# Performance work log

Hardware: AMD Instinct MI355X
Metric: run time of the kernel (lower is better)

## Reference

```python
import jax, jax.numpy as jnp
import numpy as np

# dims: P patches, D=N_azi*N_ele directions, R=P*D radiances, E COO edges,
# T echogram samples, F rfft bins
P, D, R, E, T, NOBJ = 128, 128, 16384, 131072, 1024, 8
F = T // 2 + 1
SR, C_SOUND = 16000.0, 343.0
LOG_GAMMA = float(np.log(1e-3))   # fsm_gamma = 0.001
AIR = 1e-3                        # air absorption coefficient
BOUNCES = 4                       # truncated num_bounces


def setup_inputs():
    key = jax.random.key(0)
    ks = jax.random.split(key, 11)
    return {
        "source_pos": jax.random.normal(ks[0], (3,), jnp.float32) * 2.0,
        "receiver_pos": jax.random.normal(ks[1], (3,), jnp.float32) * 2.0,
        "absorption": jax.random.uniform(ks[2], (NOBJ,), jnp.float32, minval=0.05, maxval=0.6),
        "scattering": jax.random.uniform(ks[3], (NOBJ,), jnp.float32, minval=0.1, maxval=0.9),
        "gk_val": jax.random.uniform(ks[4], (E,), jnp.float32) * 0.1,            # form factors
        "local_kernel_basis": jax.random.uniform(ks[5], (2, D, D), jnp.float32) / D,  # [brdf,Dout,Din]
        "average_distance": jax.random.uniform(ks[6], (R,), jnp.float32) * 10.0 + 1.0,  # meters
        "radiance_pos": jax.random.normal(ks[7], (R, 3), jnp.float32) * 5.0,
        "gk_row": jax.random.randint(ks[8], (E,), 0, R),
        "gk_col": jax.random.randint(ks[9], (E,), 0, R),
        "object_ids": jax.random.randint(ks[10], (P,), 0, NOBJ),
    }


def _path_factor(dist):
    """Frequency-domain factor for a propagation path of length dist [N] -> [N,F].
    Combines fractional delay phase, FSM exponential window gamma^(tau_sec),
    and air absorption exp(-alpha*dist)."""
    freqs = jnp.arange(F, dtype=jnp.float32)
    tau = dist * (SR / C_SOUND)  # delay in samples
    phase = jnp.exp((-2j * np.pi / T) * tau[:, None] * freqs[None, :])
    decay = jnp.exp((LOG_GAMMA / C_SOUND - AIR) * dist)  # fsm + air, per path
    return phase * decay[:, None].astype(phase.dtype)


def reference(source_pos, receiver_pos, absorption, scattering, gk_val,
              local_kernel_basis, average_distance, radiance_pos,
              gk_row, gk_col, object_ids):
    # --- injection: source -> patch-direction radiance [R,F] ---
    d_src = jnp.linalg.norm(radiance_pos - source_pos[None, :], axis=-1)
    g_src = 1.0 / (d_src * d_src + 1e-3)
    rad = g_src[:, None] * _path_factor(d_src)  # complex [R,F]

    # --- BRDF-factorized local kernel: K[p] = sum_b c[b,p] * B[b] ---
    refl = 1.0 - absorption                                   # [NOBJ]
    coeff = jnp.stack([refl * scattering, refl * (1.0 - scattering)])  # [2,NOBJ]
    c_patch = coeff[:, object_ids]                            # [2,P]
    K = jnp.einsum('bp,bde->pde', c_patch, local_kernel_basis)  # [P,Dout,Din]

    prop = _path_factor(average_distance)  # per-radiance transport delay/decay [R,F]

    def bounce(r):
        r = r.reshape(P, D, F)
        r = jnp.einsum('pde,pef->pdf', K.astype(jnp.complex64), r)  # local direction mixing
        r = r.reshape(R, F) * prop
        # sparse COO global kernel: out[row] += val * r[col]
        return jax.ops.segment_sum(gk_val[:, None] * r[gk_col], gk_row, num_segments=R)

    total = rad
    r = rad
    for _ in range(BOUNCES):
        r = bounce(r)
        total = total + r

    # --- detection: patch-direction radiance -> receiver echogram ---
    d_rec = jnp.linalg.norm(radiance_pos - receiver_pos[None, :], axis=-1)
    w_rec = 1.0 / (d_rec * d_rec + 1e-3)
    echo_f = jnp.sum(w_rec[:, None] * _path_factor(d_rec) * total, axis=0)  # [F]

    # FSM correction: divide out the exponential window in time domain
    t = jnp.arange(T, dtype=jnp.float32) / SR
    fsm_window = jnp.exp(LOG_GAMMA * t)
    echogram = jnp.fft.irfft(echo_f, n=T) / fsm_window
    return echogram
```

## Files before the change

### kernel.cpp

```cpp
#include <hip/hip_runtime.h>
#include <math.h>

#define PP 128
#define DD 128
#define RR 16384
#define EE 131072
#define TT 1024
#define FF 513
#define FP 520
#define FPITCH 1056
#define NRB 1024
#define PSTRIDE 528
#define EPITCH 136

#define TAU_SCALE 46.64723032069971
#define KDECAY   -0.0211392282f
#define LOG_GAMMA -6.907755278982137f
#define TWO_PI    6.283185307179586

typedef __attribute__((ext_vector_type(8))) short bf16x8;
typedef __attribute__((ext_vector_type(4))) float f32x4;
typedef unsigned short u16;

__device__ __forceinline__ u16 f2bf(float x) {
    unsigned u = __float_as_uint(x);
    unsigned r = (u + 0x7fffu + ((u >> 16) & 1u)) >> 16;
    return (u16)r;
}
__device__ __forceinline__ float bf2f(u16 b) {
    return __uint_as_float(((unsigned)b) << 16);
}

__device__ __forceinline__ void pf_sincos(float tau, int f, float* s, float* c) {
    int ti = (int)tau;
    float tf = tau - (float)ti;
    int m = (ti * f) & 1023;
    float u = fmaf(tf, (float)f, (float)m);
    float ang = u * -0.006135923151542565f;
    __sincosf(ang, s, c);
}

__global__ void k_per_row(const float* __restrict__ rpos,
                          const float* __restrict__ spos,
                          const float* __restrict__ cpos,
                          const float* __restrict__ avg_dist,
                          float* __restrict__ per_row) {
    int r = blockIdx.x * blockDim.x + threadIdx.x;
    if (r >= RR) return;
    float x = rpos[3*r], y = rpos[3*r+1], z = rpos[3*r+2];

    float dx = x - spos[0], dy = y - spos[1], dz = z - spos[2];
    float ds = sqrtf(dx*dx + dy*dy + dz*dz);
    per_row[0*RR + r] = (1.0f/(ds*ds + 0.001f)) * expf(KDECAY * ds);
    per_row[1*RR + r] = ds * (float)TAU_SCALE;

    dx = x - cpos[0]; dy = y - cpos[1]; dz = z - cpos[2];
    float dr = sqrtf(dx*dx + dy*dy + dz*dz);
    per_row[2*RR + r] = (1.0f/(dr*dr + 0.001f)) * expf(KDECAY * dr);
    per_row[3*RR + r] = dr * (float)TAU_SCALE;

    float da = avg_dist[r];
    per_row[4*RR + r] = expf(KDECAY * da);
    per_row[5*RR + r] = da * (float)TAU_SCALE;
}

__global__ void k_build_K(const float* __restrict__ absorption,
                          const float* __restrict__ scattering,
                          const int* __restrict__ object_ids,
                          const float* __restrict__ basis,
                          float* __restrict__ Kmat) {
    int idx = blockIdx.x * 256 + threadIdx.x;
    int p  = idx >> 14;
    int de = idx & 16383;
    int obj = object_ids[p];
    float refl = 1.0f - absorption[obj];
    float sc   = scattering[obj];
    Kmat[idx] = refl*sc*basis[de] + refl*(1.0f - sc)*basis[16384 + de];
}

__global__ void k_count(const int* __restrict__ gk_row, int* __restrict__ counts) {
    int e = blockIdx.x * 256 + threadIdx.x;
    atomicAdd(&counts[gk_row[e]], 1);
}

__global__ __launch_bounds__(1024) void k_scan(const int* __restrict__ counts,
                                               int* __restrict__ row_start,
                                               int* __restrict__ cursor) {
    __shared__ int sh[1024];
    int tid = threadIdx.x;
    int base = tid * 16;
    int local[16];
    int sum = 0;
    #pragma unroll
    for (int j = 0; j < 16; j++) { local[j] = sum; sum += counts[base + j]; }
    sh[tid] = sum;
    __syncthreads();
    for (int off = 1; off < 1024; off <<= 1) {
        int v = (tid >= off) ? sh[tid - off] : 0;
        __syncthreads();
        sh[tid] += v;
        __syncthreads();
    }
    int chunk_excl = sh[tid] - sum;
    #pragma unroll
    for (int j = 0; j < 16; j++) {
        int v = chunk_excl + local[j];
        row_start[base + j] = v;
        cursor[base + j] = v;
    }
    if (tid == 1023) row_start[RR] = chunk_excl + sum;
}

__global__ void k_scatter(const int* __restrict__ gk_row,
                          const float* __restrict__ gk_val,
                          const int* __restrict__ gk_col,
                          int* __restrict__ cursor,
                          int2* __restrict__ edge) {
    int e = blockIdx.x * 256 + threadIdx.x;
    int pos = atomicAdd(&cursor[gk_row[e]], 1);
    edge[pos] = make_int2(gk_col[e], __float_as_int(gk_val[e]));
}

__global__ __launch_bounds__(256) void k_init(const float* __restrict__ per_row,
                                              u16* __restrict__ cur,
                                              float* __restrict__ echo) {
    __shared__ float2 sh[4][64][9];
    int fl = threadIdx.x & 63, rg = threadIdx.x >> 6;
    int r0 = blockIdx.x * 32;
    float2 eacc[9];
    #pragma unroll
    for (int k = 0; k < 9; k++) eacc[k] = make_float2(0.f, 0.f);

    for (int i = 0; i < 8; i++) {
        int r = r0 + rg + i * 4;
        float amp = per_row[r],      tau  = per_row[RR + r];
        float w   = per_row[2*RR+r], taur = per_row[3*RR + r];
        float s1, c1, rs1, rc1, s2, c2, rs2, rc2;
        pf_sincos(tau,  fl, &s1, &c1);  pf_sincos(tau,  64, &rs1, &rc1);
        pf_sincos(taur, fl, &s2, &c2);  pf_sincos(taur, 64, &rs2, &rc2);
        u16* wrow = cur + (size_t)r * FPITCH;
        #pragma unroll
        for (int k = 0; k < 9; k++) {
            int f = fl + (k << 6);
            float re = amp * c1, im = amp * s1;
            if (f < FP)
                *(unsigned*)(wrow + f * 2) =
                    (unsigned)f2bf(re) | ((unsigned)f2bf(im) << 16);
            if (f < FF) {
                eacc[k].x = fmaf(w, c2*re - s2*im, eacc[k].x);
                eacc[k].y = fmaf(w, c2*im + s2*re, eacc[k].y);
            }
            float n1c = c1*rc1 - s1*rs1, n1s = s1*rc1 + c1*rs1;
            c1 = n1c; s1 = n1s;
            float n2c = c2*rc2 - s2*rs2, n2s = s2*rc2 + c2*rs2;
            c2 = n2c; s2 = n2s;
        }
    }
    #pragma unroll
    for (int k = 0; k < 9; k++) sh[rg][fl][k] = eacc[k];
    __syncthreads();
    if (rg == 0) {
        #pragma unroll
        for (int k = 0; k < 9; k++) {
            int f = fl + (k << 6);
            if (f < FF) {
                float sx = sh[0][fl][k].x + sh[1][fl][k].x + sh[2][fl][k].x + sh[3][fl][k].x;
                float sy = sh[0][fl][k].y + sh[1][fl][k].y + sh[2][fl][k].y + sh[3][fl][k].y;
                atomicAdd(&echo[2*f],   sx);
                atomicAdd(&echo[2*f+1], sy);
            }
        }
    }
}

__global__ __launch_bounds__(256) void k_matmul(const float* __restrict__ Kmat,
                                                const u16* __restrict__ in,
                                                const float* __restrict__ per_row,
                                                u16* __restrict__ out) {
    __shared__ u16 vlds[2][16 * EPITCH];
    int b = blockIdx.x;
    int xcd = b & 7;
    int g = b >> 3;
    int p = (g >> 3) * 8 + xcd;
    int nq = g & 7;
    int nt0 = nq * 8;
    int ntEnd = (nq == 7) ? 65 : nt0 + 8;

    int tid  = threadIdx.x;
    int wave = tid >> 6;
    int lane = tid & 63;
    int quad = lane >> 4;
    int n    = lane & 15;
    int mt0  = wave << 1;

    bf16x8 Ah[2][4], Al[2][4];
    #pragma unroll
    for (int mi = 0; mi < 2; mi++) {
        const float* kp = Kmat + (p << 14) + ((mt0 + mi) * 16 + n) * 128 + quad * 8;
        #pragma unroll
        for (int kt = 0; kt < 4; kt++) {
            float4 x0 = *(const float4*)(kp + kt * 32);
            float4 x1 = *(const float4*)(kp + kt * 32 + 4);
            float xs[8] = {x0.x,x0.y,x0.z,x0.w,x1.x,x1.y,x1.z,x1.w};
            bf16x8 h, l;
            #pragma unroll
            for (int j = 0; j < 8; j++) {
                u16 hb = f2bf(xs[j]);
                h[j] = (short)hb;
                l[j] = (short)f2bf(xs[j] - bf2f(hb));
            }
            Ah[mi][kt] = h; Al[mi][kt] = l;
        }
    }
    float dec_[2][4];
    float pc[2][4], ps[2][4];
    float rc[2][4], rs[2][4];
    int fq = (n >> 1);
    #pragma unroll
    for (int mi = 0; mi < 2; mi++)
        #pragma unroll
        for (int r = 0; r < 4; r++) {
            int row = (p << 7) + (mt0 + mi) * 16 + quad * 4 + r;
            dec_[mi][r] = per_row[4*RR + row];
            float tau = per_row[5*RR + row];
            pf_sincos(tau, nt0 * 8 + fq, &ps[mi][r], &pc[mi][r]);
            pf_sincos(tau, 8, &rs[mi][r], &rc[mi][r]);
        }

    const u16* pin = in + (size_t)(p << 7) * FPITCH;
    uint4 pk;
    int se = tid >> 1, sc8 = (tid & 1) << 3;
    auto loadTile = [&](int nt) {
        pk = *(const uint4*)(pin + (size_t)se * FPITCH + nt * 16 + sc8);
    };
    auto writeTile = [&](int buf) {
        u16* dst = &vlds[buf][0];
        unsigned w[4] = {pk.x, pk.y, pk.z, pk.w};
        #pragma unroll
        for (int j = 0; j < 8; j++) {
            u16 v = (u16)(w[j >> 1] >> ((j & 1) * 16));
            dst[(sc8 + j) * EPITCH + se] = v;
        }
    };

    loadTile(nt0); writeTile(0);
    for (int nt = nt0; nt < ntEnd; nt++) {
        int cb = (nt - nt0) & 1;
        __syncthreads();
        if (nt + 1 < ntEnd) { loadTile(nt + 1); writeTile(cb ^ 1); }

        f32x4 acc0 = {0.f,0.f,0.f,0.f}, acc1 = {0.f,0.f,0.f,0.f};
        const u16* vb = &vlds[cb][n * EPITCH];
        #pragma unroll
        for (int kt = 0; kt < 4; kt++) {
            bf16x8 Bh = *(const bf16x8*)(vb + kt * 32 + quad * 8);
            acc0 = __builtin_amdgcn_mfma_f32_16x16x32_bf16(Ah[0][kt], Bh, acc0, 0,0,0);
            acc1 = __builtin_amdgcn_mfma_f32_16x16x32_bf16(Ah[1][kt], Bh, acc1, 0,0,0);
            acc0 = __builtin_amdgcn_mfma_f32_16x16x32_bf16(Al[0][kt], Bh, acc0, 0,0,0);
            acc1 = __builtin_amdgcn_mfma_f32_16x16x32_bf16(Al[1][kt], Bh, acc1, 0,0,0);
        }

        int nfl = nt * 16 + n;
        bool odd = nfl & 1;
        #pragma unroll
        for (int mi = 0; mi < 2; mi++) {
            f32x4 a = mi ? acc1 : acc0;
            #pragma unroll
            for (int r = 0; r < 4; r++) {
                float av = a[r];
                float pv = __shfl_xor(av, 1);
                float s = ps[mi][r], c = pc[mi][r];
                float o = dec_[mi][r] * (odd ? fmaf(av, c,  s*pv)
                                             : fmaf(av, c, -s*pv));
                int row = (p << 7) + (mt0 + mi) * 16 + quad * 4 + r;
                out[(size_t)row * FPITCH + nfl] = f2bf(o);
                float nc = c*rc[mi][r] - s*rs[mi][r];
                float nsv = s*rc[mi][r] + c*rs[mi][r];
                pc[mi][r] = nc; ps[mi][r] = nsv;
            }
        }
    }
}

__global__ __launch_bounds__(512) void k_segsum(const int* __restrict__ row_start,
                                                const int2* __restrict__ edge,
                                                const u16* __restrict__ in,
                                                u16* __restrict__ outp,
                                                const float* __restrict__ per_row,
                                                float2* __restrict__ part,
                                                int store_cur) {
    __shared__ float2 sh[4][128][5];
    int rb = blockIdx.x;
    int fl = threadIdx.x & 127, ry = threadIdx.x >> 7;
    bool tail = (fl < 8);
    float2 e0 = {0.f,0.f}, e1 = {0.f,0.f}, e2 = {0.f,0.f}, e3 = {0.f,0.f}, e4 = {0.f,0.f};

    for (int i = 0; i < 4; i++) {
        int row = (rb << 4) + (ry << 2) + i;
        int s0 = row_start[row], s1 = row_start[row + 1];
        float a0r=0.f,a0i=0.f,a1r=0.f,a1i=0.f,a2r=0.f,a2i=0.f,a3r=0.f,a3i=0.f;
        float t4r=0.f,t4i=0.f;
        int t = s0;
        for (; t + 1 < s1; t += 2) {
            int2 ed0 = edge[t], ed1 = edge[t+1];
            float v0 = __int_as_float(ed0.y), v1 = __int_as_float(ed1.y);
            const u16* g0p = in + (size_t)ed0.x * FPITCH + (fl << 1);
            const u16* g1p = in + (size_t)ed1.x * FPITCH + (fl << 1);
            unsigned b00 = *(const unsigned*)(g0p);
            unsigned b01 = *(const unsigned*)(g0p + 256);
            unsigned b02 = *(const unsigned*)(g0p + 512);
            unsigned b03 = *(const unsigned*)(g0p + 768);
            unsigned b10 = *(const unsigned*)(g1p);
            unsigned b11 = *(const unsigned*)(g1p + 256);
            unsigned b12 = *(const unsigned*)(g1p + 512);
            unsigned b13 = *(const unsigned*)(g1p + 768);
            a0r = fmaf(v0, bf2f((u16)(b00 & 0xffffu)), a0r); a0i = fmaf(v0, bf2f((u16)(b00 >> 16)), a0i);
            a1r = fmaf(v0, bf2f((u16)(b01 & 0xffffu)), a1r); a1i = fmaf(v0, bf2f((u16)(b01 >> 16)), a1i);
            a2r = fmaf(v0, bf2f((u16)(b02 & 0xffffu)), a2r); a2i = fmaf(v0, bf2f((u16)(b02 >> 16)), a2i);
            a3r = fmaf(v0, bf2f((u16)(b03 & 0xffffu)), a3r); a3i = fmaf(v0, bf2f((u16)(b03 >> 16)), a3i);
            a0r = fmaf(v1, bf2f((u16)(b10 & 0xffffu)), a0r); a0i = fmaf(v1, bf2f((u16)(b10 >> 16)), a0i);
            a1r = fmaf(v1, bf2f((u16)(b11 & 0xffffu)), a1r); a1i = fmaf(v1, bf2f((u16)(b11 >> 16)), a1i);
            a2r = fmaf(v1, bf2f((u16)(b12 & 0xffffu)), a2r); a2i = fmaf(v1, bf2f((u16)(b12 >> 16)), a2i);
            a3r = fmaf(v1, bf2f((u16)(b13 & 0xffffu)), a3r); a3i = fmaf(v1, bf2f((u16)(b13 >> 16)), a3i);
            if (tail) {
                unsigned b04 = *(const unsigned*)(g0p + 1024);
                unsigned b14 = *(const unsigned*)(g1p + 1024);
                t4r = fmaf(v0, bf2f((u16)(b04 & 0xffffu)), t4r); t4i = fmaf(v0, bf2f((u16)(b04 >> 16)), t4i);
                t4r = fmaf(v1, bf2f((u16)(b14 & 0xffffu)), t4r); t4i = fmaf(v1, bf2f((u16)(b14 >> 16)), t4i);
            }
        }
        if (t < s1) {
            int2 ed = edge[t];
            float v = __int_as_float(ed.y);
            const u16* g = in + (size_t)ed.x * FPITCH + (fl << 1);
            unsigned b0 = *(const unsigned*)(g);
            unsigned b1 = *(const unsigned*)(g + 256);
            unsigned b2 = *(const unsigned*)(g + 512);
            unsigned b3 = *(const unsigned*)(g + 768);
            a0r = fmaf(v, bf2f((u16)(b0 & 0xffffu)), a0r); a0i = fmaf(v, bf2f((u16)(b0 >> 16)), a0i);
            a1r = fmaf(v, bf2f((u16)(b1 & 0xffffu)), a1r); a1i = fmaf(v, bf2f((u16)(b1 >> 16)), a1i);
            a2r = fmaf(v, bf2f((u16)(b2 & 0xffffu)), a2r); a2i = fmaf(v, bf2f((u16)(b2 >> 16)), a2i);
            a3r = fmaf(v, bf2f((u16)(b3 & 0xffffu)), a3r); a3i = fmaf(v, bf2f((u16)(b3 >> 16)), a3i);
            if (tail) {
                unsigned b4 = *(const unsigned*)(g + 1024);
                t4r = fmaf(v, bf2f((u16)(b4 & 0xffffu)), t4r); t4i = fmaf(v, bf2f((u16)(b4 >> 16)), t4i);
            }
        }
        if (store_cur) {
            u16* w = outp + (size_t)row * FPITCH + (fl << 1);
            *(unsigned*)(w)       = (unsigned)f2bf(a0r) | ((unsigned)f2bf(a0i) << 16);
            *(unsigned*)(w + 256) = (unsigned)f2bf(a1r) | ((unsigned)f2bf(a1i) << 16);
            *(unsigned*)(w + 512) = (unsigned)f2bf(a2r) | ((unsigned)f2bf(a2i) << 16);
            *(unsigned*)(w + 768) = (unsigned)f2bf(a3r) | ((unsigned)f2bf(a3i) << 16);
            if (tail)
                *(unsigned*)(w + 1024) = (unsigned)f2bf(t4r) | ((unsigned)f2bf(t4i) << 16);
        }
        float wr = per_row[2*RR + row], taur = per_row[3*RR + row];
        float s, c;
        pf_sincos(taur, fl, &s, &c);
        e0.x = fmaf(wr, c*a0r - s*a0i, e0.x); e0.y = fmaf(wr, c*a0i + s*a0r, e0.y);
        pf_sincos(taur, fl + 128, &s, &c);
        e1.x = fmaf(wr, c*a1r - s*a1i, e1.x); e1.y = fmaf(wr, c*a1i + s*a1r, e1.y);
        pf_sincos(taur, fl + 256, &s, &c);
        e2.x = fmaf(wr, c*a2r - s*a2i, e2.x); e2.y = fmaf(wr, c*a2i + s*a2r, e2.y);
        pf_sincos(taur, fl + 384, &s, &c);
        e3.x = fmaf(wr, c*a3r - s*a3i, e3.x); e3.y = fmaf(wr, c*a3i + s*a3r, e3.y);
        if (tail && (512 + fl) < FF) {
            pf_sincos(taur, 512 + fl, &s, &c);
            e4.x = fmaf(wr, c*t4r - s*t4i, e4.x); e4.y = fmaf(wr, c*t4i + s*t4r, e4.y);
        }
    }
    sh[ry][fl][0] = e0; sh[ry][fl][1] = e1; sh[ry][fl][2] = e2;
    sh[ry][fl][3] = e3; sh[ry][fl][4] = e4;
    __syncthreads();
    if (ry == 0) {
        float2* pp = part + (size_t)rb * PSTRIDE;
        #pragma unroll
        for (int sidx = 0; sidx < 5; sidx++) {
            int fidx = sidx * 128 + fl;
            if (fidx < FP) {
                float2 v0 = sh[0][fl][sidx], v1 = sh[1][fl][sidx];
                float2 v2 = sh[2][fl][sidx], v3 = sh[3][fl][sidx];
                float2 acc = pp[fidx];
                acc.x += v0.x + v1.x + v2.x + v3.x;
                acc.y += v0.y + v1.y + v2.y + v3.y;
                pp[fidx] = acc;
            }
        }
    }
}

__global__ __launch_bounds__(256) void k_fold(const float2* __restrict__ part,
                                              float* __restrict__ echo) {
    int f = blockIdx.x;
    float sx = 0.f, sy = 0.f;
    for (int rb = threadIdx.x; rb < NRB; rb += 256) {
        float2 v = part[(size_t)rb * PSTRIDE + f];
        sx += v.x; sy += v.y;
    }
    for (int off = 32; off >= 1; off >>= 1) {
        sx += __shfl_down(sx, off, 64);
        sy += __shfl_down(sy, off, 64);
    }
    __shared__ float red[2][4];
    int lane = threadIdx.x & 63, w = threadIdx.x >> 6;
    if (lane == 0) { red[0][w] = sx; red[1][w] = sy; }
    __syncthreads();
    if (threadIdx.x == 0) {
        sx = red[0][0]+red[0][1]+red[0][2]+red[0][3];
        sy = red[1][0]+red[1][1]+red[1][2]+red[1][3];
        echo[2*f] += sx;
        echo[2*f+1] += sy;
    }
}

__global__ void k_irfft(const float* __restrict__ echo, float* __restrict__ out) {
    int t = blockIdx.x * blockDim.x + threadIdx.x;
    float acc = echo[0];
    float nyq = echo[2 * 512];
    acc += (t & 1) ? -nyq : nyq;
    for (int f = 1; f < 512; f++) {
        int m = (f * t) & 1023;
        float ang = (float)m * 0.006135923151542565f;
        float s, c; __sincosf(ang, &s, &c);
        acc += 2.0f * (echo[2*f]*c - echo[2*f+1]*s);
    }
    acc *= (1.0f / 1024.0f);
    float tsec = (float)t * (1.0f / 16000.0f);
    float win = expf(LOG_GAMMA * tsec);
    out[t] = acc / win;
}

extern "C" void kernel_launch(void* const* d_in, const int* in_sizes, int n_in,
                              void* d_out, int out_size, void* d_ws, size_t ws_size,
                              hipStream_t stream) {
    const float* source_pos   = (const float*)d_in[0];
    const float* receiver_pos = (const float*)d_in[1];
    const float* absorption   = (const float*)d_in[2];
    const float* scattering   = (const float*)d_in[3];
    const float* gk_val       = (const float*)d_in[4];
    const float* basis        = (const float*)d_in[5];
    const float* avg_dist     = (const float*)d_in[6];
    const float* rpos         = (const float*)d_in[7];
    const int*   gk_row       = (const int*)d_in[8];
    const int*   gk_col       = (const int*)d_in[9];
    const int*   object_ids   = (const int*)d_in[10];
    float* out = (float*)d_out;

    char* base = (char*)d_ws;
    size_t off = 0;
    auto alloc = [&](size_t bytes) -> void* {
        void* ptr = base + off;
        off = (off + bytes + 255) & ~(size_t)255;
        return ptr;
    };
    const size_t PLANE = (size_t)RR * FPITCH + FPITCH;
    float*  Kmat      = (float*)alloc(sizeof(float) * PP * DD * DD);
    u16*    cur       = (u16*)alloc(sizeof(u16) * PLANE);
    u16*    nxt       = (u16*)alloc(sizeof(u16) * PLANE);
    float*  per_row   = (float*)alloc(sizeof(float) * 6 * RR);
    int*    counts    = (int*)alloc(sizeof(int) * RR);
    int*    row_start = (int*)alloc(sizeof(int) * (RR + 1));
    int*    cursor    = (int*)alloc(sizeof(int) * RR);
    int2*   edge      = (int2*)alloc(sizeof(int2) * EE);
    float2* part      = (float2*)alloc(sizeof(float2) * NRB * PSTRIDE);
    float*  echo      = (float*)alloc(sizeof(float) * 1056);

    hipMemsetAsync(counts, 0, sizeof(int) * RR, stream);
    hipMemsetAsync(echo, 0, sizeof(float) * 1056, stream);
    hipMemsetAsync(part, 0, sizeof(float2) * NRB * PSTRIDE, stream);

    k_per_row<<<RR / 256, 256, 0, stream>>>(rpos, source_pos, receiver_pos, avg_dist, per_row);
    k_build_K<<<(PP * DD * DD) / 256, 256, 0, stream>>>(absorption, scattering, object_ids, basis, Kmat);
    k_count<<<EE / 256, 256, 0, stream>>>(gk_row, counts);
    k_scan<<<1, 1024, 0, stream>>>(counts, row_start, cursor);
    k_scatter<<<EE / 256, 256, 0, stream>>>(gk_row, gk_val, gk_col, cursor, edge);
    k_init<<<512, 256, 0, stream>>>(per_row, cur, echo);

    for (int b = 0; b < 4; b++) {
        k_matmul<<<1024, 256, 0, stream>>>(Kmat, cur, per_row, nxt);
        k_segsum<<<NRB, 512, 0, stream>>>(row_start, edge, nxt, cur,
                                          per_row, part, (b < 3) ? 1 : 0);
    }

    k_fold<<<FF, 256, 0, stream>>>(part, echo);
    k_irfft<<<4, 256, 0, stream>>>(echo, out);
}
```

Before: 485.3 us.

## Degree-sort rows for segsum, split frequencies across blocks, double-tile matmul stages

Rows are bucketed by edge count (histogram, scan, scatter), and the segment-sum kernel walks them in that order so rows with similar work share a block. Each block now covers 128 rows and one 64-bin slice of frequencies, where it used to cover 16 rows across all bins. NRB drops to 128, which shrinks the partials buffer and the fold work. The matmul kernel stages two N-tiles per barrier to halve synchronisations. This adds three small setup kernels, narrower per-thread gathers, and a serial 32-row shared reduction per block.

```diff
diff --git a/kernel.cpp b/kernel.cpp
--- a/kernel.cpp
+++ b/kernel.cpp
@@ -9,7 +9,7 @@
 #define FF 513
 #define FP 520
 #define FPITCH 1056
-#define NRB 1024
+#define NRB 128
 #define PSTRIDE 528
 #define EPITCH 136
 
@@ -121,6 +121,27 @@
     edge[pos] = make_int2(gk_col[e], __float_as_int(gk_val[e]));
 }
 
+__global__ void k_hist(const int* __restrict__ counts, int* __restrict__ bins) {
+    int r = blockIdx.x * 256 + threadIdx.x;
+    int c = counts[r]; if (c > 255) c = 255;
+    atomicAdd(&bins[c], 1);
+}
+__global__ __launch_bounds__(256) void k_binscan(const int* __restrict__ bins,
+                                                 int* __restrict__ bin_cursor) {
+    int t = threadIdx.x;
+    int s = 0;
+    for (int c = t + 1; c < 256; c++) s += bins[c];
+    bin_cursor[t] = s;
+}
+__global__ void k_scatter_rows(const int* __restrict__ counts,
+                               int* __restrict__ bin_cursor,
+                               int* __restrict__ row_order) {
+    int r = blockIdx.x * 256 + threadIdx.x;
+    int c = counts[r]; if (c > 255) c = 255;
+    int pos = atomicAdd(&bin_cursor[c], 1);
+    row_order[pos] = r;
+}
+
 __global__ __launch_bounds__(256) void k_init(const float* __restrict__ per_row,
                                               u16* __restrict__ cur,
                                               float* __restrict__ echo) {
@@ -177,7 +198,7 @@
                                                 const u16* __restrict__ in,
                                                 const float* __restrict__ per_row,
                                                 u16* __restrict__ out) {
-    __shared__ u16 vlds[2][16 * EPITCH];
+    __shared__ u16 vlds[2][32 * EPITCH];
     int b = blockIdx.x;
     int xcd = b & 7;
     int g = b >> 3;
@@ -185,6 +206,7 @@
     int nq = g & 7;
     int nt0 = nq * 8;
     int ntEnd = (nq == 7) ? 65 : nt0 + 8;
+    int nStages = (ntEnd - nt0 + 1) >> 1;
 
     int tid  = threadIdx.x;
     int wave = tid >> 6;
@@ -228,55 +250,62 @@
         }
 
     const u16* pin = in + (size_t)(p << 7) * FPITCH;
-    uint4 pk;
-    int se = tid >> 1, sc8 = (tid & 1) << 3;
-    auto loadTile = [&](int nt) {
-        pk = *(const uint4*)(pin + (size_t)se * FPITCH + nt * 16 + sc8);
+    uint4 pk0, pk1;
+    int se = tid >> 1, sc16 = (tid & 1) << 4;
+    auto loadStage = [&](int st) {
+        const u16* src = pin + (size_t)se * FPITCH + (nt0 + 2*st) * 16 + sc16;
+        pk0 = *(const uint4*)(src);
+        pk1 = *(const uint4*)(src + 8);
     };
-    auto writeTile = [&](int buf) {
+    auto writeStage = [&](int buf) {
         u16* dst = &vlds[buf][0];
-        unsigned w[4] = {pk.x, pk.y, pk.z, pk.w};
-        #pragma unroll
-        for (int j = 0; j < 8; j++) {
+        unsigned w[8] = {pk0.x, pk0.y, pk0.z, pk0.w, pk1.x, pk1.y, pk1.z, pk1.w};
+        #pragma unroll
+        for (int j = 0; j < 16; j++) {
             u16 v = (u16)(w[j >> 1] >> ((j & 1) * 16));
-            dst[(sc8 + j) * EPITCH + se] = v;
+            dst[(sc16 + j) * EPITCH + se] = v;
         }
     };
 
-    loadTile(nt0); writeTile(0);
-    for (int nt = nt0; nt < ntEnd; nt++) {
-        int cb = (nt - nt0) & 1;
+    loadStage(0); writeStage(0);
+    for (int st = 0; st < nStages; st++) {
+        int cb = st & 1;
         __syncthreads();
-        if (nt + 1 < ntEnd) { loadTile(nt + 1); writeTile(cb ^ 1); }
-
-        f32x4 acc0 = {0.f,0.f,0.f,0.f}, acc1 = {0.f,0.f,0.f,0.f};
-        const u16* vb = &vlds[cb][n * EPITCH];
-        #pragma unroll
-        for (int kt = 0; kt < 4; kt++) {
-            bf16x8 Bh = *(const bf16x8*)(vb + kt * 32 + quad * 8);
-            acc0 = __builtin_amdgcn_mfma_f32_16x16x32_bf16(Ah[0][kt], Bh, acc0, 0,0,0);
-            acc1 = __builtin_amdgcn_mfma_f32_16x16x32_bf16(Ah[1][kt], Bh, acc1, 0,0,0);
-            acc0 = __builtin_amdgcn_mfma_f32_16x16x32_bf16(Al[0][kt], Bh, acc0, 0,0,0);
-            acc1 = __builtin_amdgcn_mfma_f32_16x16x32_bf16(Al[1][kt], Bh, acc1, 0,0,0);
-        }
-
-        int nfl = nt * 16 + n;
-        bool odd = nfl & 1;
-        #pragma unroll
-        for (int mi = 0; mi < 2; mi++) {
-            f32x4 a = mi ? acc1 : acc0;
+        if (st + 1 < nStages) { loadStage(st + 1); writeStage(cb ^ 1); }
+
+        #pragma unroll
+        for (int sub = 0; sub < 2; sub++) {
+            int nt = nt0 + 2*st + sub;
+            if (nt >= ntEnd) break;
+            f32x4 acc0 = {0.f,0.f,0.f,0.f}, acc1 = {0.f,0.f,0.f,0.f};
+            const u16* vb = &vlds[cb][(n + (sub << 4)) * EPITCH];
             #pragma unroll
-            for (int r = 0; r < 4; r++) {
-                float av = a[r];
-                float pv = __shfl_xor(av, 1);
-                float s = ps[mi][r], c = pc[mi][r];
-                float o = dec_[mi][r] * (odd ? fmaf(av, c,  s*pv)
-                                             : fmaf(av, c, -s*pv));
-                int row = (p << 7) + (mt0 + mi) * 16 + quad * 4 + r;
-                out[(size_t)row * FPITCH + nfl] = f2bf(o);
-                float nc = c*rc[mi][r] - s*rs[mi][r];
-                float nsv = s*rc[mi][r] + c*rs[mi][r];
-                pc[mi][r] = nc; ps[mi][r] = nsv;
+            for (int kt = 0; kt < 4; kt++) {
+                bf16x8 Bh = *(const bf16x8*)(vb + kt * 32 + quad * 8);
+                acc0 = __builtin_amdgcn_mfma_f32_16x16x32_bf16(Ah[0][kt], Bh, acc0, 0,0,0);
+                acc1 = __builtin_amdgcn_mfma_f32_16x16x32_bf16(Ah[1][kt], Bh, acc1, 0,0,0);
+                acc0 = __builtin_amdgcn_mfma_f32_16x16x32_bf16(Al[0][kt], Bh, acc0, 0,0,0);
+                acc1 = __builtin_amdgcn_mfma_f32_16x16x32_bf16(Al[1][kt], Bh, acc1, 0,0,0);
+            }
+
+            int nfl = nt * 16 + n;
+            bool odd = nfl & 1;
+            #pragma unroll
+            for (int mi = 0; mi < 2; mi++) {
+                f32x4 a = mi ? acc1 : acc0;
+                #pragma unroll
+                for (int r = 0; r < 4; r++) {
+                    float av = a[r];
+                    float pv = __shfl_xor(av, 1);
+                    float s = ps[mi][r], c = pc[mi][r];
+                    float o = dec_[mi][r] * (odd ? fmaf(av, c,  s*pv)
+                                                 : fmaf(av, c, -s*pv));
+                    int row = (p << 7) + (mt0 + mi) * 16 + quad * 4 + r;
+                    out[(size_t)row * FPITCH + nfl] = f2bf(o);
+                    float nc = c*rc[mi][r] - s*rs[mi][r];
+                    float nsv = s*rc[mi][r] + c*rs[mi][r];
+                    pc[mi][r] = nc; ps[mi][r] = nsv;
+                }
             }
         }
     }
@@ -288,105 +317,114 @@
                                                 u16* __restrict__ outp,
                                                 const float* __restrict__ per_row,
                                                 float2* __restrict__ part,
+                                                const int* __restrict__ row_order,
                                                 int store_cur) {
-    __shared__ float2 sh[4][128][5];
-    int rb = blockIdx.x;
-    int fl = threadIdx.x & 127, ry = threadIdx.x >> 7;
-    bool tail = (fl < 8);
-    float2 e0 = {0.f,0.f}, e1 = {0.f,0.f}, e2 = {0.f,0.f}, e3 = {0.f,0.f}, e4 = {0.f,0.f};
+    __shared__ float2 sh[32][16][4];
+    __shared__ float2 sht[32][8];
+    int c  = blockIdx.x & 7;
+    int rb = blockIdx.x >> 3;
+    int fl = threadIdx.x & 15;
+    int rl = threadIdx.x >> 4;
+    int fbase = (c << 6) + fl;
+    bool tl = (c == 7) && (fl < 8);
+    float2 ech[4];
+    #pragma unroll
+    for (int k = 0; k < 4; k++) ech[k] = make_float2(0.f, 0.f);
+    float2 echt = make_float2(0.f, 0.f);
 
     for (int i = 0; i < 4; i++) {
-        int row = (rb << 4) + (ry << 2) + i;
+        int row = row_order[(rb << 7) + (rl << 2) + i];
         int s0 = row_start[row], s1 = row_start[row + 1];
-        float a0r=0.f,a0i=0.f,a1r=0.f,a1i=0.f,a2r=0.f,a2i=0.f,a3r=0.f,a3i=0.f;
-        float t4r=0.f,t4i=0.f;
+        float ar[4], ai[4]; float tr = 0.f, ti = 0.f;
+        #pragma unroll
+        for (int k = 0; k < 4; k++) { ar[k] = 0.f; ai[k] = 0.f; }
         int t = s0;
         for (; t + 1 < s1; t += 2) {
-            int2 ed0 = edge[t], ed1 = edge[t+1];
-            float v0 = __int_as_float(ed0.y), v1 = __int_as_float(ed1.y);
-            const u16* g0p = in + (size_t)ed0.x * FPITCH + (fl << 1);
-            const u16* g1p = in + (size_t)ed1.x * FPITCH + (fl << 1);
-            unsigned b00 = *(const unsigned*)(g0p);
-            unsigned b01 = *(const unsigned*)(g0p + 256);
-            unsigned b02 = *(const unsigned*)(g0p + 512);
-            unsigned b03 = *(const unsigned*)(g0p + 768);
-            unsigned b10 = *(const unsigned*)(g1p);
-            unsigned b11 = *(const unsigned*)(g1p + 256);
-            unsigned b12 = *(const unsigned*)(g1p + 512);
-            unsigned b13 = *(const unsigned*)(g1p + 768);
-            a0r = fmaf(v0, bf2f((u16)(b00 & 0xffffu)), a0r); a0i = fmaf(v0, bf2f((u16)(b00 >> 16)), a0i);
-            a1r = fmaf(v0, bf2f((u16)(b01 & 0xffffu)), a1r); a1i = fmaf(v0, bf2f((u16)(b01 >> 16)), a1i);
-            a2r = fmaf(v0, bf2f((u16)(b02 & 0xffffu)), a2r); a2i = fmaf(v0, bf2f((u16)(b02 >> 16)), a2i);
-            a3r = fmaf(v0, bf2f((u16)(b03 & 0xffffu)), a3r); a3i = fmaf(v0, bf2f((u16)(b03 >> 16)), a3i);
-            a0r = fmaf(v1, bf2f((u16)(b10 & 0xffffu)), a0r); a0i = fmaf(v1, bf2f((u16)(b10 >> 16)), a0i);
-            a1r = fmaf(v1, bf2f((u16)(b11 & 0xffffu)), a1r); a1i = fmaf(v1, bf2f((u16)(b11 >> 16)), a1i);
-            a2r = fmaf(v1, bf2f((u16)(b12 & 0xffffu)), a2r); a2i = fmaf(v1, bf2f((u16)(b12 >> 16)), a2i);
-            a3r = fmaf(v1, bf2f((u16)(b13 & 0xffffu)), a3r); a3i = fmaf(v1, bf2f((u16)(b13 >> 16)), a3i);
-            if (tail) {
-                unsigned b04 = *(const unsigned*)(g0p + 1024);
-                unsigned b14 = *(const unsigned*)(g1p + 1024);
-                t4r = fmaf(v0, bf2f((u16)(b04 & 0xffffu)), t4r); t4i = fmaf(v0, bf2f((u16)(b04 >> 16)), t4i);
-                t4r = fmaf(v1, bf2f((u16)(b14 & 0xffffu)), t4r); t4i = fmaf(v1, bf2f((u16)(b14 >> 16)), t4i);
+            int2 e0 = edge[t], e1 = edge[t+1];
+            float v0 = __int_as_float(e0.y), v1 = __int_as_float(e1.y);
+            const u16* g0 = in + (size_t)e0.x * FPITCH + (fbase << 1);
+            const u16* g1 = in + (size_t)e1.x * FPITCH + (fbase << 1);
+            unsigned b00 = *(const unsigned*)(g0);
+            unsigned b01 = *(const unsigned*)(g0 + 32);
+            unsigned b02 = *(const unsigned*)(g0 + 64);
+            unsigned b03 = *(const unsigned*)(g0 + 96);
+            unsigned b10 = *(const unsigned*)(g1);
+            unsigned b11 = *(const unsigned*)(g1 + 32);
+            unsigned b12 = *(const unsigned*)(g1 + 64);
+            unsigned b13 = *(const unsigned*)(g1 + 96);
+            ar[0] = fmaf(v0, bf2f((u16)(b00 & 0xffffu)), ar[0]); ai[0] = fmaf(v0, bf2f((u16)(b00 >> 16)), ai[0]);
+            ar[1] = fmaf(v0, bf2f((u16)(b01 & 0xffffu)), ar[1]); ai[1] = fmaf(v0, bf2f((u16)(b01 >> 16)), ai[1]);
+            ar[2] = fmaf(v0, bf2f((u16)(b02 & 0xffffu)), ar[2]); ai[2] = fmaf(v0, bf2f((u16)(b02 >> 16)), ai[2]);
+            ar[3] = fmaf(v0, bf2f((u16)(b03 & 0xffffu)), ar[3]); ai[3] = fmaf(v0, bf2f((u16)(b03 >> 16)), ai[3]);
+            ar[0] = fmaf(v1, bf2f((u16)(b10 & 0xffffu)), ar[0]); ai[0] = fmaf(v1, bf2f((u16)(b10 >> 16)), ai[0]);
+            ar[1] = fmaf(v1, bf2f((u16)(b11 & 0xffffu)), ar[1]); ai[1] = fmaf(v1, bf2f((u16)(b11 >> 16)), ai[1]);
+            ar[2] = fmaf(v1, bf2f((u16)(b12 & 0xffffu)), ar[2]); ai[2] = fmaf(v1, bf2f((u16)(b12 >> 16)), ai[2]);
+            ar[3] = fmaf(v1, bf2f((u16)(b13 & 0xffffu)), ar[3]); ai[3] = fmaf(v1, bf2f((u16)(b13 >> 16)), ai[3]);
+            if (tl) {
+                unsigned b04 = *(const unsigned*)(in + (size_t)e0.x * FPITCH + 1024 + (fl << 1));
+                unsigned b14 = *(const unsigned*)(in + (size_t)e1.x * FPITCH + 1024 + (fl << 1));
+                tr = fmaf(v0, bf2f((u16)(b04 & 0xffffu)), tr); ti = fmaf(v0, bf2f((u16)(b04 >> 16)), ti);
+                tr = fmaf(v1, bf2f((u16)(b14 & 0xffffu)), tr); ti = fmaf(v1, bf2f((u16)(b14 >> 16)), ti);
             }
         }
         if (t < s1) {
             int2 ed = edge[t];
             float v = __int_as_float(ed.y);
-            const u16* g = in + (size_t)ed.x * FPITCH + (fl << 1);
+            const u16* g = in + (size_t)ed.x * FPITCH + (fbase << 1);
             unsigned b0 = *(const unsigned*)(g);
-            unsigned b1 = *(const unsigned*)(g + 256);
-            unsigned b2 = *(const unsigned*)(g + 512);
-            unsigned b3 = *(const unsigned*)(g + 768);
-            a0r = fmaf(v, bf2f((u16)(b0 & 0xffffu)), a0r); a0i = fmaf(v, bf2f((u16)(b0 >> 16)), a0i);
-            a1r = fmaf(v, bf2f((u16)(b1 & 0xffffu)), a1r); a1i = fmaf(v, bf2f((u16)(b1 >> 16)), a1i);
-            a2r = fmaf(v, bf2f((u16)(b2 & 0xffffu)), a2r); a2i = fmaf(v, bf2f((u16)(b2 >> 16)), a2i);
-            a3r = fmaf(v, bf2f((u16)(b3 & 0xffffu)), a3r); a3i = fmaf(v, bf2f((u16)(b3 >> 16)), a3i);
-            if (tail) {
-                unsigned b4 = *(const unsigned*)(g + 1024);
-                t4r = fmaf(v, bf2f((u16)(b4 & 0xffffu)), t4r); t4i = fmaf(v, bf2f((u16)(b4 >> 16)), t4i);
+            unsigned b1 = *(const unsigned*)(g + 32);
+            unsigned b2 = *(const unsigned*)(g + 64);
+            unsigned b3 = *(const unsigned*)(g + 96);
+            ar[0] = fmaf(v, bf2f((u16)(b0 & 0xffffu)), ar[0]); ai[0] = fmaf(v, bf2f((u16)(b0 >> 16)), ai[0]);
+            ar[1] = fmaf(v, bf2f((u16)(b1 & 0xffffu)), ar[1]); ai[1] = fmaf(v, bf2f((u16)(b1 >> 16)), ai[1]);
+            ar[2] = fmaf(v, bf2f((u16)(b2 & 0xffffu)), ar[2]); ai[2] = fmaf(v, bf2f((u16)(b2 >> 16)), ai[2]);
+            ar[3] = fmaf(v, bf2f((u16)(b3 & 0xffffu)), ar[3]); ai[3] = fmaf(v, bf2f((u16)(b3 >> 16)), ai[3]);
+            if (tl) {
+                unsigned b4 = *(const unsigned*)(in + (size_t)ed.x * FPITCH + 1024 + (fl << 1));
+                tr = fmaf(v, bf2f((u16)(b4 & 0xffffu)), tr); ti = fmaf(v, bf2f((u16)(b4 >> 16)), ti);
             }
         }
         if (store_cur) {
-            u16* w = outp + (size_t)row * FPITCH + (fl << 1);
-            *(unsigned*)(w)       = (unsigned)f2bf(a0r) | ((unsigned)f2bf(a0i) << 16);
-            *(unsigned*)(w + 256) = (unsigned)f2bf(a1r) | ((unsigned)f2bf(a1i) << 16);
-            *(unsigned*)(w + 512) = (unsigned)f2bf(a2r) | ((unsigned)f2bf(a2i) << 16);
-            *(unsigned*)(w + 768) = (unsigned)f2bf(a3r) | ((unsigned)f2bf(a3i) << 16);
-            if (tail)
-                *(unsigned*)(w + 1024) = (unsigned)f2bf(t4r) | ((unsigned)f2bf(t4i) << 16);
+            u16* w = outp + (size_t)row * FPITCH + (fbase << 1);
+            *(unsigned*)(w)      = (unsigned)f2bf(ar[0]) | ((unsigned)f2bf(ai[0]) << 16);
+            *(unsigned*)(w + 32) = (unsigned)f2bf(ar[1]) | ((unsigned)f2bf(ai[1]) << 16);
+            *(unsigned*)(w + 64) = (unsigned)f2bf(ar[2]) | ((unsigned)f2bf(ai[2]) << 16);
+            *(unsigned*)(w + 96) = (unsigned)f2bf(ar[3]) | ((unsigned)f2bf(ai[3]) << 16);
+            if (tl)
+                *(unsigned*)(outp + (size_t)row * FPITCH + 1024 + (fl << 1)) =
+                    (unsigned)f2bf(tr) | ((unsigned)f2bf(ti) << 16);
         }
         float wr = per_row[2*RR + row], taur = per_row[3*RR + row];
-        float s, c;
-        pf_sincos(taur, fl, &s, &c);
-        e0.x = fmaf(wr, c*a0r - s*a0i, e0.x); e0.y = fmaf(wr, c*a0i + s*a0r, e0.y);
-        pf_sincos(taur, fl + 128, &s, &c);
-        e1.x = fmaf(wr, c*a1r - s*a1i, e1.x); e1.y = fmaf(wr, c*a1i + s*a1r, e1.y);
-        pf_sincos(taur, fl + 256, &s, &c);
-        e2.x = fmaf(wr, c*a2r - s*a2i, e2.x); e2.y = fmaf(wr, c*a2i + s*a2r, e2.y);
-        pf_sincos(taur, fl + 384, &s, &c);
-        e3.x = fmaf(wr, c*a3r - s*a3i, e3.x); e3.y = fmaf(wr, c*a3i + s*a3r, e3.y);
-        if (tail && (512 + fl) < FF) {
-            pf_sincos(taur, 512 + fl, &s, &c);
-            e4.x = fmaf(wr, c*t4r - s*t4i, e4.x); e4.y = fmaf(wr, c*t4i + s*t4r, e4.y);
-        }
-    }
-    sh[ry][fl][0] = e0; sh[ry][fl][1] = e1; sh[ry][fl][2] = e2;
-    sh[ry][fl][3] = e3; sh[ry][fl][4] = e4;
+        #pragma unroll
+        for (int k = 0; k < 4; k++) {
+            float s, cc; pf_sincos(taur, fbase + (k << 4), &s, &cc);
+            ech[k].x = fmaf(wr, cc*ar[k] - s*ai[k], ech[k].x);
+            ech[k].y = fmaf(wr, cc*ai[k] + s*ar[k], ech[k].y);
+        }
+        if (tl && (512 + fl) < FF) {
+            float s, cc; pf_sincos(taur, 512 + fl, &s, &cc);
+            echt.x = fmaf(wr, cc*tr - s*ti, echt.x);
+            echt.y = fmaf(wr, cc*ti + s*tr, echt.y);
+        }
+    }
+    #pragma unroll
+    for (int k = 0; k < 4; k++) sh[rl][fl][k] = ech[k];
+    if (tl) sht[rl][fl] = echt;
     __syncthreads();
-    if (ry == 0) {
-        float2* pp = part + (size_t)rb * PSTRIDE;
-        #pragma unroll
-        for (int sidx = 0; sidx < 5; sidx++) {
-            int fidx = sidx * 128 + fl;
-            if (fidx < FP) {
-                float2 v0 = sh[0][fl][sidx], v1 = sh[1][fl][sidx];
-                float2 v2 = sh[2][fl][sidx], v3 = sh[3][fl][sidx];
-                float2 acc = pp[fidx];
-                acc.x += v0.x + v1.x + v2.x + v3.x;
-                acc.y += v0.y + v1.y + v2.y + v3.y;
-                pp[fidx] = acc;
-            }
-        }
+    int tid = threadIdx.x;
+    if (tid < 64) {
+        int k = tid >> 4, f16 = tid & 15;
+        int f = (c << 6) + f16 + (k << 4);
+        float sx = 0.f, sy = 0.f;
+        for (int r = 0; r < 32; r++) { sx += sh[r][f16][k].x; sy += sh[r][f16][k].y; }
+        float2* pp = part + (size_t)rb * PSTRIDE + f;
+        float2 acc = *pp; acc.x += sx; acc.y += sy; *pp = acc;
+    } else if (c == 7 && tid < 72) {
+        int flt = tid - 64;
+        float sx = 0.f, sy = 0.f;
+        for (int r = 0; r < 32; r++) { sx += sht[r][flt].x; sy += sht[r][flt].y; }
+        float2* pp = part + (size_t)rb * PSTRIDE + 512 + flt;
+        float2 acc = *pp; acc.x += sx; acc.y += sy; *pp = acc;
     }
 }
 
@@ -465,22 +503,29 @@
     int2*   edge      = (int2*)alloc(sizeof(int2) * EE);
     float2* part      = (float2*)alloc(sizeof(float2) * NRB * PSTRIDE);
     float*  echo      = (float*)alloc(sizeof(float) * 1056);
+    int*    bins      = (int*)alloc(sizeof(int) * 256);
+    int*    bin_cur   = (int*)alloc(sizeof(int) * 256);
+    int*    row_order = (int*)alloc(sizeof(int) * RR);
 
     hipMemsetAsync(counts, 0, sizeof(int) * RR, stream);
     hipMemsetAsync(echo, 0, sizeof(float) * 1056, stream);
     hipMemsetAsync(part, 0, sizeof(float2) * NRB * PSTRIDE, stream);
+    hipMemsetAsync(bins, 0, sizeof(int) * 256, stream);
 
     k_per_row<<<RR / 256, 256, 0, stream>>>(rpos, source_pos, receiver_pos, avg_dist, per_row);
     k_build_K<<<(PP * DD * DD) / 256, 256, 0, stream>>>(absorption, scattering, object_ids, basis, Kmat);
     k_count<<<EE / 256, 256, 0, stream>>>(gk_row, counts);
     k_scan<<<1, 1024, 0, stream>>>(counts, row_start, cursor);
     k_scatter<<<EE / 256, 256, 0, stream>>>(gk_row, gk_val, gk_col, cursor, edge);
+    k_hist<<<RR / 256, 256, 0, stream>>>(counts, bins);
+    k_binscan<<<1, 256, 0, stream>>>(bins, bin_cur);
+    k_scatter_rows<<<RR / 256, 256, 0, stream>>>(counts, bin_cur, row_order);
     k_init<<<512, 256, 0, stream>>>(per_row, cur, echo);
 
     for (int b = 0; b < 4; b++) {
         k_matmul<<<1024, 256, 0, stream>>>(Kmat, cur, per_row, nxt);
-        k_segsum<<<NRB, 512, 0, stream>>>(row_start, edge, nxt, cur,
-                                          per_row, part, (b < 3) ? 1 : 0);
+        k_segsum<<<1024, 512, 0, stream>>>(row_start, edge, nxt, cur,
+                                           per_row, part, row_order, (b < 3) ? 1 : 0);
     }
 
     k_fold<<<FF, 256, 0, stream>>>(part, echo);
```

New measurement: 642.0 us. 1.32x slower.

## Split complex tiles into separate real/imag LDS planes in matmul kernel

Applied to the files above, without the earlier changes.

The k_matmul kernel now deinterleaves each complex input tile into separate real and imaginary LDS buffers. Each tile step processes 16 full complex frequencies instead of 16 interleaved scalars, so the phase rotation no longer needs a cross-lane shuffle and the output is written as packed re/im 32-bit stores. Each tile iteration issues twice as many MFMAs over half as many iterations, and the injection kernel now writes padding up to 528 frequencies so the last 16-wide tile reads initialized data. This trades the shuffle and odd/even branch for doubled LDS footprint and more register pressure from four accumulators.

```diff
diff --git a/kernel.cpp b/kernel.cpp
--- a/kernel.cpp
+++ b/kernel.cpp
@@ -8,6 +8,7 @@
 #define TT 1024
 #define FF 513
 #define FP 520
+#define FPW 528
 #define FPITCH 1056
 #define NRB 1024
 #define PSTRIDE 528
@@ -143,7 +144,7 @@
         for (int k = 0; k < 9; k++) {
             int f = fl + (k << 6);
             float re = amp * c1, im = amp * s1;
-            if (f < FP)
+            if (f < FPW)
                 *(unsigned*)(wrow + f * 2) =
                     (unsigned)f2bf(re) | ((unsigned)f2bf(im) << 16);
             if (f < FF) {
@@ -177,14 +178,15 @@
                                                 const u16* __restrict__ in,
                                                 const float* __restrict__ per_row,
                                                 u16* __restrict__ out) {
-    __shared__ u16 vlds[2][16 * EPITCH];
+    __shared__ u16 relds[2][16 * EPITCH];
+    __shared__ u16 imlds[2][16 * EPITCH];
     int b = blockIdx.x;
     int xcd = b & 7;
     int g = b >> 3;
     int p = (g >> 3) * 8 + xcd;
-    int nq = g & 7;
-    int nt0 = nq * 8;
-    int ntEnd = (nq == 7) ? 65 : nt0 + 8;
+    int q = g & 7;
+    int ct0 = q * 4;
+    int ctEnd = (q == 7) ? 33 : ct0 + 4;
 
     int tid  = threadIdx.x;
     int wave = tid >> 6;
@@ -215,7 +217,6 @@
     float dec_[2][4];
     float pc[2][4], ps[2][4];
     float rc[2][4], rs[2][4];
-    int fq = (n >> 1);
     #pragma unroll
     for (int mi = 0; mi < 2; mi++)
         #pragma unroll
@@ -223,57 +224,67 @@
             int row = (p << 7) + (mt0 + mi) * 16 + quad * 4 + r;
             dec_[mi][r] = per_row[4*RR + row];
             float tau = per_row[5*RR + row];
-            pf_sincos(tau, nt0 * 8 + fq, &ps[mi][r], &pc[mi][r]);
-            pf_sincos(tau, 8, &rs[mi][r], &rc[mi][r]);
+            pf_sincos(tau, ct0 * 16 + n, &ps[mi][r], &pc[mi][r]);
+            pf_sincos(tau, 16, &rs[mi][r], &rc[mi][r]);
         }
 
     const u16* pin = in + (size_t)(p << 7) * FPITCH;
-    uint4 pk;
-    int se = tid >> 1, sc8 = (tid & 1) << 3;
-    auto loadTile = [&](int nt) {
-        pk = *(const uint4*)(pin + (size_t)se * FPITCH + nt * 16 + sc8);
+    uint4 pk0, pk1;
+    int se = tid >> 1, h = tid & 1;
+    auto loadTile = [&](int ct) {
+        const u16* src = pin + (size_t)se * FPITCH + ct * 32 + h * 16;
+        pk0 = *(const uint4*)(src);
+        pk1 = *(const uint4*)(src + 8);
     };
     auto writeTile = [&](int buf) {
-        u16* dst = &vlds[buf][0];
-        unsigned w[4] = {pk.x, pk.y, pk.z, pk.w};
-        #pragma unroll
-        for (int j = 0; j < 8; j++) {
-            u16 v = (u16)(w[j >> 1] >> ((j & 1) * 16));
-            dst[(sc8 + j) * EPITCH + se] = v;
+        unsigned w[8] = {pk0.x, pk0.y, pk0.z, pk0.w, pk1.x, pk1.y, pk1.z, pk1.w};
+        int cbase = h * 8;
+        #pragma unroll
+        for (int k = 0; k < 8; k++) {
+            int col = cbase + k;
+            relds[buf][col * EPITCH + se] = (u16)(w[k] & 0xffffu);
+            imlds[buf][col * EPITCH + se] = (u16)(w[k] >> 16);
         }
     };
 
-    loadTile(nt0); writeTile(0);
-    for (int nt = nt0; nt < ntEnd; nt++) {
-        int cb = (nt - nt0) & 1;
+    loadTile(ct0); writeTile(0);
+    for (int ct = ct0; ct < ctEnd; ct++) {
+        int cb = (ct - ct0) & 1;
         __syncthreads();
-        if (nt + 1 < ntEnd) { loadTile(nt + 1); writeTile(cb ^ 1); }
-
-        f32x4 acc0 = {0.f,0.f,0.f,0.f}, acc1 = {0.f,0.f,0.f,0.f};
-        const u16* vb = &vlds[cb][n * EPITCH];
+        if (ct + 1 < ctEnd) { loadTile(ct + 1); writeTile(cb ^ 1); }
+
+        f32x4 ar0 = {0.f,0.f,0.f,0.f}, ar1 = {0.f,0.f,0.f,0.f};
+        f32x4 ai0 = {0.f,0.f,0.f,0.f}, ai1 = {0.f,0.f,0.f,0.f};
+        const u16* vr = &relds[cb][n * EPITCH];
+        const u16* vi = &imlds[cb][n * EPITCH];
         #pragma unroll
         for (int kt = 0; kt < 4; kt++) {
-            bf16x8 Bh = *(const bf16x8*)(vb + kt * 32 + quad * 8);
-            acc0 = __builtin_amdgcn_mfma_f32_16x16x32_bf16(Ah[0][kt], Bh, acc0, 0,0,0);
-            acc1 = __builtin_amdgcn_mfma_f32_16x16x32_bf16(Ah[1][kt], Bh, acc1, 0,0,0);
-            acc0 = __builtin_amdgcn_mfma_f32_16x16x32_bf16(Al[0][kt], Bh, acc0, 0,0,0);
-            acc1 = __builtin_amdgcn_mfma_f32_16x16x32_bf16(Al[1][kt], Bh, acc1, 0,0,0);
-        }
-
-        int nfl = nt * 16 + n;
-        bool odd = nfl & 1;
+            bf16x8 Br = *(const bf16x8*)(vr + kt * 32 + quad * 8);
+            bf16x8 Bi = *(const bf16x8*)(vi + kt * 32 + quad * 8);
+            ar0 = __builtin_amdgcn_mfma_f32_16x16x32_bf16(Ah[0][kt], Br, ar0, 0,0,0);
+            ar1 = __builtin_amdgcn_mfma_f32_16x16x32_bf16(Ah[1][kt], Br, ar1, 0,0,0);
+            ai0 = __builtin_amdgcn_mfma_f32_16x16x32_bf16(Ah[0][kt], Bi, ai0, 0,0,0);
+            ai1 = __builtin_amdgcn_mfma_f32_16x16x32_bf16(Ah[1][kt], Bi, ai1, 0,0,0);
+            ar0 = __builtin_amdgcn_mfma_f32_16x16x32_bf16(Al[0][kt], Br, ar0, 0,0,0);
+            ar1 = __builtin_amdgcn_mfma_f32_16x16x32_bf16(Al[1][kt], Br, ar1, 0,0,0);
+            ai0 = __builtin_amdgcn_mfma_f32_16x16x32_bf16(Al[0][kt], Bi, ai0, 0,0,0);
+            ai1 = __builtin_amdgcn_mfma_f32_16x16x32_bf16(Al[1][kt], Bi, ai1, 0,0,0);
+        }
+
+        int f = ct * 16 + n;
         #pragma unroll
         for (int mi = 0; mi < 2; mi++) {
-            f32x4 a = mi ? acc1 : acc0;
+            f32x4 are = mi ? ar1 : ar0;
+            f32x4 aim = mi ? ai1 : ai0;
             #pragma unroll
             for (int r = 0; r < 4; r++) {
-                float av = a[r];
-                float pv = __shfl_xor(av, 1);
+                float re = are[r], im = aim[r];
                 float s = ps[mi][r], c = pc[mi][r];
-                float o = dec_[mi][r] * (odd ? fmaf(av, c,  s*pv)
-                                             : fmaf(av, c, -s*pv));
+                float ore = dec_[mi][r] * (c*re - s*im);
+                float oim = dec_[mi][r] * (c*im + s*re);
                 int row = (p << 7) + (mt0 + mi) * 16 + quad * 4 + r;
-                out[(size_t)row * FPITCH + nfl] = f2bf(o);
+                *(unsigned*)(out + (size_t)row * FPITCH + f * 2) =
+                    (unsigned)f2bf(ore) | ((unsigned)f2bf(oim) << 16);
                 float nc = c*rc[mi][r] - s*rs[mi][r];
                 float nsv = s*rc[mi][r] + c*rs[mi][r];
                 pc[mi][r] = nc; ps[mi][r] = nsv;
```

New measurement: 477.9 us. Within noise of the previous version (-1.5%).
